# Kernel tuning notes

Hardware: AMD Instinct MI355X
Metric: run time of the kernel (lower is better)

Reference implementation:

```python
import jax, jax.numpy as jnp
import numpy as np

BIT = 64
M_MARGIN = 2.0 * BIT  # m = 2 * bit
ALPHA = 0.1
N_TRAIN = 100000
N_CLASSES = 100
BATCH = 512


def setup_inputs() -> dict:
    key = jax.random.key(0)
    k1, k2, k3, k4 = jax.random.split(key, 4)
    u = jax.random.normal(k1, (BATCH, BIT), dtype=jnp.float32)
    y = jax.random.randint(k2, (BATCH, N_CLASSES), 0, 2).astype(jnp.float32)
    ind = jnp.arange(BATCH, dtype=jnp.int32)
    U = jax.random.normal(k3, (N_TRAIN, BIT), dtype=jnp.float32)
    Y = jax.random.randint(k4, (N_TRAIN, N_CLASSES), 0, 2).astype(jnp.float32)
    return {"u": u, "y": y, "ind": ind, "U": U, "Y": Y}


def reference(u, y, ind, U, Y):
    # Buffer updates (torch uses u.data / y.float(): detached writes)
    U = U.at[ind].set(jax.lax.stop_gradient(u))  # [N, bit]
    Y = Y.at[ind].set(jax.lax.stop_gradient(y))  # [N, C]

    # Pairwise squared L2 distances via the expansion identity (same math as
    # (u[:,None]-U[None]).pow(2).sum(-1) but without the [B,N,bit] intermediate)
    u_sq = jnp.sum(u * u, axis=1, keepdims=True)        # [B, 1]
    U_sq = jnp.sum(U * U, axis=1)[None, :]              # [1, N]
    dist = jnp.maximum(u_sq - 2.0 * (u @ U.T) + U_sq, 0.0)  # [B, N]

    # match mask: 1 where labels share no class (y @ Y.T == 0)
    mismatch = (y @ Y.T == 0).astype(u.dtype)           # [B, N]

    loss = (1.0 - mismatch) * 0.5 * dist + mismatch * 0.5 * jnp.maximum(M_MARGIN - dist, 0.0)
    loss1 = loss.mean()
    loss2 = ALPHA * jnp.abs(1.0 - jnp.sign(u)).mean()
    return loss1 + loss2
```

## Files before the change

### kernel.cpp

```cpp
#include <hip/hip_runtime.h>
#include <stdint.h>

#define NTRAIN 100000
#define BATCH  512
#define BIT    64
#define NCLS   100
#define MARGINF 128.0f

#define CHUNK  256
#define NSCAN  ((NTRAIN + CHUNK - 1) / CHUNK)
#define NCORR  8
#define NGU    2
#define NUS    2
#define LISTCAP 1024

#define YMP_OFF   0
#define YMO_OFF   8192
#define MISS_OFF  16384
#define ACC_OFF   24576
#define CNT_OFF   25600
#define LIST_OFF  25664

typedef unsigned long long u64;

__device__ __forceinline__ uint4 row_mask(const float* __restrict__ row) {
  const float4* r4 = (const float4*)row;
  unsigned w0 = 0, w1 = 0, w2 = 0, w3 = 0;
#pragma unroll
  for (int j = 0; j < NCLS / 4; ++j) {
    float4 v = r4[j];
    int bp = (4 * j) & 31;
    unsigned m = ((v.x != 0.f) ? 1u : 0u) << bp
               | ((v.y != 0.f) ? 2u : 0u) << bp
               | ((v.z != 0.f) ? 4u : 0u) << bp
               | ((v.w != 0.f) ? 8u : 0u) << bp;
    int word = (4 * j) >> 5;
    if (word == 0) w0 |= m; else if (word == 1) w1 |= m;
    else if (word == 2) w2 |= m; else w3 |= m;
  }
  return make_uint4(w0, w1, w2, w3);
}

__device__ __forceinline__ float pair_term(const float* __restrict__ a,
                                           const float* __restrict__ c) {
  const float4* a4 = (const float4*)a;
  const float4* c4 = (const float4*)c;
  float usq = 0.f, Usq = 0.f, uv = 0.f;
#pragma unroll
  for (int k = 0; k < BIT / 4; ++k) {
    float4 x = a4[k], z = c4[k];
    usq = fmaf(x.x, x.x, fmaf(x.y, x.y, fmaf(x.z, x.z, fmaf(x.w, x.w, usq))));
    Usq = fmaf(z.x, z.x, fmaf(z.y, z.y, fmaf(z.z, z.z, fmaf(z.w, z.w, Usq))));
    uv  = fmaf(x.x, z.x, fmaf(x.y, z.y, fmaf(x.z, z.z, fmaf(x.w, z.w, uv))));
  }
  float d = usq + Usq - 2.f * uv;
  float dc = fmaxf(d, 0.f);
  return 0.5f * fmaxf(MARGINF - dc, 0.f) - 0.5f * d;
}

__global__ void __launch_bounds__(64) k_prep(const float* __restrict__ y,
                                             const float* __restrict__ Y,
                                             const int* __restrict__ ind,
                                             uint4* __restrict__ ymaskp,
                                             uint4* __restrict__ ymold,
                                             u64* __restrict__ missg,
                                             float* __restrict__ accf,
                                             int* __restrict__ listcnt) {
  int bid = blockIdx.x, t = threadIdx.x;
  if (bid < 8) {
    int b = bid * 64 + t;
    uint4 ym = row_mask(y + (size_t)b * NCLS);
    ymaskp[b] = ym;
    ymold[b]  = row_mask(Y + (size_t)ind[b] * NCLS);
#pragma unroll
    for (int c = 0; c < NCLS; ++c) {
      unsigned word = (c < 32) ? ym.x : (c < 64) ? ym.y : (c < 96) ? ym.z : ym.w;
      unsigned bit = (word >> (c & 31)) & 1u;
      u64 bal = __ballot(bit == 0u);
      if (t == 0) missg[c * 8 + bid] = bal;
    }
  } else {
    for (int i = t; i < 144; i += 64) accf[i] = 0.0f;
    if (t == 0) *listcnt = 0;
  }
}

__global__ void __launch_bounds__(512) k_main(
    const float4* __restrict__ U4, const float* __restrict__ Uf,
    const float* __restrict__ Y,
    const float4* __restrict__ u4, const float* __restrict__ u,
    const int* __restrict__ ind,
    const uint4* __restrict__ ymaskp, const uint4* __restrict__ ymold,
    const u64* __restrict__ missg,
    float* __restrict__ accf, int* __restrict__ listcnt, int* __restrict__ list) {
  __shared__ uint4 masks[CHUNK];
  __shared__ u64 mlds[NCLS * 9];
  __shared__ float colred[4][64];
  __shared__ float sqred[4];
  int bid = blockIdx.x, t = threadIdx.x;
  int w = t >> 6, l = t & 63;

  if (bid < NSCAN) {
    int n0 = bid * CHUNK;
    int nvalid = min(CHUNK, NTRAIN - n0);
    if (w < 4) {
      masks[t] = (t < nvalid) ? row_mask(Y + (size_t)(n0 + t) * NCLS)
                              : make_uint4(0u, 0u, 0u, 0u);
    } else {
      for (int i = t - 256; i < NCLS * 8; i += 256)
        mlds[(i >> 3) * 9 + (i & 7)] = missg[i];
      float s0 = 0, s1 = 0, s2 = 0, s3 = 0, sq = 0;
      for (int f = t - 256; f < nvalid * (BIT / 4); f += 256) {
        float4 v = U4[(size_t)n0 * (BIT / 4) + f];
        s0 += v.x; s1 += v.y; s2 += v.z; s3 += v.w;
        sq = fmaf(v.x, v.x, fmaf(v.y, v.y, fmaf(v.z, v.z, fmaf(v.w, v.w, sq))));
      }
      s0 += __shfl_xor(s0, 16); s0 += __shfl_xor(s0, 32);
      s1 += __shfl_xor(s1, 16); s1 += __shfl_xor(s1, 32);
      s2 += __shfl_xor(s2, 16); s2 += __shfl_xor(s2, 32);
      s3 += __shfl_xor(s3, 16); s3 += __shfl_xor(s3, 32);
      for (int off = 32; off; off >>= 1) sq += __shfl_xor(sq, off);
      int ww = w - 4;
      if (l < 16) { colred[ww][l * 4 + 0] = s0; colred[ww][l * 4 + 1] = s1;
                    colred[ww][l * 4 + 2] = s2; colred[ww][l * 4 + 3] = s3; }
      if (l == 0) sqred[ww] = sq;
    }
    __syncthreads();
    if (w == 0) {
      atomicAdd(&accf[l], colred[0][l] + colred[1][l] + colred[2][l] + colred[3][l]);
      if (l == 0) atomicAdd(&accf[128], sqred[0] + sqred[1] + sqred[2] + sqred[3]);
    }
    int grp = t >> 3;
    int g   = t & 7;
#pragma unroll
    for (int k = 0; k < CHUNK / 64; ++k) {
      int n_local = grp + 64 * k;
      bool alive = n_local < nvalid;
      uint4 ym = masks[n_local];
      u64 rem0 = (u64)ym.x | ((u64)ym.y << 32);
      u64 rem1 = (u64)ym.z | ((u64)ym.w << 32);
      u64 acc = alive ? ~0ull : 0ull;
      while (__ballot((acc != 0ull) && ((rem0 | rem1) != 0ull)) != 0ull) {
#pragma unroll
        for (int kk = 0; kk < 4; ++kk) {
          int c = -1;
          if (rem0) { c = __builtin_ctzll(rem0); rem0 &= rem0 - 1ull; }
          else if (rem1) { c = 64 + __builtin_ctzll(rem1); rem1 &= rem1 - 1ull; }
          u64 mm = mlds[(c >= 0 ? c : 0) * 9 + g];
          if (c >= 0) acc &= mm;
        }
      }
      u64 mbal = __ballot(acc != 0ull);
      if (g == 0 && ((mbal >> (8 * (grp & 7))) & 0xffull)) {
        int idx = atomicAdd(listcnt, 1);
        if (idx < LISTCAP) list[idx] = n0 + n_local;
      }
    }
  } else if (bid < NSCAN + NCORR) {
    int cb = bid - NSCAN;
    uint4 ym = ymaskp[t];
    float corr = 0.f;
    for (int j = 0; j < 64; ++j) {
      int bp = cb * 64 + j;
      uint4 mo = ymold[bp];
      uint4 mn = ymaskp[bp];
      unsigned a = (ym.x & mo.x) | (ym.y & mo.y) | (ym.z & mo.z) | (ym.w & mo.w);
      unsigned c = (ym.x & mn.x) | (ym.y & mn.y) | (ym.z & mn.z) | (ym.w & mn.w);
      if (__builtin_expect(__ballot((a == 0u) | (c == 0u)) != 0ull, 0)) {
        const float* ub = u + (size_t)t * BIT;
        if (a == 0u) corr -= pair_term(ub, Uf + (size_t)ind[bp] * BIT);
        if (c == 0u) corr += pair_term(ub, u + (size_t)bp * BIT);
      }
    }
    if (corr != 0.f) atomicAdd(&accf[131], corr);
  } else if (bid < NSCAN + NCORR + NGU) {
    int gb = bid - NSCAN - NCORR;
    float s0 = 0, s1 = 0, s2 = 0, s3 = 0, sq = 0;
    for (int f = t; f < 256 * (BIT / 4); f += 512) {
      int r = gb * 256 + (f >> 4);
      float4 v = U4[(size_t)ind[r] * (BIT / 4) + (f & 15)];
      s0 += v.x; s1 += v.y; s2 += v.z; s3 += v.w;
      sq = fmaf(v.x, v.x, fmaf(v.y, v.y, fmaf(v.z, v.z, fmaf(v.w, v.w, sq))));
    }
    s0 += __shfl_xor(s0, 16); s0 += __shfl_xor(s0, 32);
    s1 += __shfl_xor(s1, 16); s1 += __shfl_xor(s1, 32);
    s2 += __shfl_xor(s2, 16); s2 += __shfl_xor(s2, 32);
    s3 += __shfl_xor(s3, 16); s3 += __shfl_xor(s3, 32);
    for (int off = 32; off; off >>= 1) sq += __shfl_xor(sq, off);
    int c4 = l & 15;
    if (l < 16) {
      atomicAdd(&accf[c4 * 4 + 0], -s0); atomicAdd(&accf[c4 * 4 + 1], -s1);
      atomicAdd(&accf[c4 * 4 + 2], -s2); atomicAdd(&accf[c4 * 4 + 3], -s3);
    }
    if (l == 0) atomicAdd(&accf[128], -sq);
  } else {
    int gb = bid - NSCAN - NCORR - NGU;
    float s0 = 0, s1 = 0, s2 = 0, s3 = 0, sq = 0, sg = 0;
    for (int f = t; f < 256 * (BIT / 4); f += 512) {
      float4 v = u4[(size_t)gb * 256 * (BIT / 4) + f];
      s0 += v.x; s1 += v.y; s2 += v.z; s3 += v.w;
      sq = fmaf(v.x, v.x, fmaf(v.y, v.y, fmaf(v.z, v.z, fmaf(v.w, v.w, sq))));
      sg += ((v.x < 0.f) ? 2.f : (v.x == 0.f) ? 1.f : 0.f)
          + ((v.y < 0.f) ? 2.f : (v.y == 0.f) ? 1.f : 0.f)
          + ((v.z < 0.f) ? 2.f : (v.z == 0.f) ? 1.f : 0.f)
          + ((v.w < 0.f) ? 2.f : (v.w == 0.f) ? 1.f : 0.f);
    }
    s0 += __shfl_xor(s0, 16); s0 += __shfl_xor(s0, 32);
    s1 += __shfl_xor(s1, 16); s1 += __shfl_xor(s1, 32);
    s2 += __shfl_xor(s2, 16); s2 += __shfl_xor(s2, 32);
    s3 += __shfl_xor(s3, 16); s3 += __shfl_xor(s3, 32);
    for (int off = 32; off; off >>= 1) { sq += __shfl_xor(sq, off); sg += __shfl_xor(sg, off); }
    int c4 = l & 15;
    if (l < 16) {
      atomicAdd(&accf[64 + c4 * 4 + 0], s0); atomicAdd(&accf[64 + c4 * 4 + 1], s1);
      atomicAdd(&accf[64 + c4 * 4 + 2], s2); atomicAdd(&accf[64 + c4 * 4 + 3], s3);
    }
    if (l == 0) { atomicAdd(&accf[129], sq); atomicAdd(&accf[130], sg); }
  }
}

__global__ void __launch_bounds__(512) k_finalfix(
    const float* __restrict__ Y, const float* __restrict__ u, const float* __restrict__ Uf,
    const uint4* __restrict__ ymaskp, const int* __restrict__ listcnt,
    const int* __restrict__ list, float* __restrict__ accf, float* __restrict__ out) {
  int t = threadIdx.x;
  int cnt = min(*listcnt, LISTCAP);
  if (__builtin_expect(cnt > 0, 0)) {
    uint4 ymb = ymaskp[t];
    float corr = 0.f;
    for (int i = 0; i < cnt; ++i) {
      int n = list[i];
      uint4 Ym = row_mask(Y + (size_t)n * NCLS);
      unsigned m = (ymb.x & Ym.x) | (ymb.y & Ym.y) | (ymb.z & Ym.z) | (ymb.w & Ym.w);
      if (m == 0u) corr += pair_term(u + (size_t)t * BIT, Uf + (size_t)n * BIT);
    }
    if (corr != 0.f) atomicAdd(&accf[131], corr);
  }
  __syncthreads();
  if (t < 64) {
    double dotp = (double)accf[t] * (double)accf[64 + t];
    for (int off = 32; off; off >>= 1) dotp += __shfl_down(dotp, off);
    if (t == 0) {
      double S_Usq = accf[128];
      double s_usq = accf[129];
      double sg    = accf[130];
      double corr  = accf[131];
      double sum_dist = (double)NTRAIN * s_usq + (double)BATCH * S_Usq - 2.0 * dotp;
      double loss1 = (0.5 * sum_dist + corr) / ((double)BATCH * (double)NTRAIN);
      double loss2 = 0.1 * sg / ((double)BATCH * (double)BIT);
      out[0] = (float)(loss1 + loss2);
    }
  }
}

extern "C" void kernel_launch(void* const* d_in, const int* in_sizes, int n_in,
                              void* d_out, int out_size, void* d_ws, size_t ws_size,
                              hipStream_t stream) {
  const float* u   = (const float*)d_in[0];
  const float* y   = (const float*)d_in[1];
  const int*   ind = (const int*)d_in[2];
  const float* U   = (const float*)d_in[3];
  const float* Y   = (const float*)d_in[4];
  uint4* ymaskp = (uint4*)((char*)d_ws + YMP_OFF);
  uint4* ymold  = (uint4*)((char*)d_ws + YMO_OFF);
  u64*   missg  = (u64*)((char*)d_ws + MISS_OFF);
  float* accf   = (float*)((char*)d_ws + ACC_OFF);
  int*   cnt    = (int*)((char*)d_ws + CNT_OFF);
  int*   list   = (int*)((char*)d_ws + LIST_OFF);
  float* out    = (float*)d_out;

  hipLaunchKernelGGL(k_prep, dim3(9), dim3(64), 0, stream,
                     y, Y, ind, ymaskp, ymold, missg, accf, cnt);
  hipLaunchKernelGGL(k_main, dim3(NSCAN + NCORR + NGU + NUS), dim3(512), 0, stream,
                     (const float4*)U, U, Y, (const float4*)u, u, ind,
                     ymaskp, ymold, missg, accf, cnt, list);
  hipLaunchKernelGGL(k_finalfix, dim3(1), dim3(512), 0, stream,
                     Y, u, U, ymaskp, cnt, list, accf, out);
}
```

Before: 127.9 us.

## Coalesce label-mask building with shared-memory atomicOr across all threads

Label bitmasks are now built cooperatively: each thread reads one contiguous float4 of the label matrix and ORs a nibble into a shared-memory mask word, replacing per-row strided loads done by one thread per row. In the main scan kernel all 8 waves now share both the mask build and the U column-sum work, and the prep kernel becomes 2 blocks of 512 threads. The aim is coalesced global reads of Y and better load balance. The cost is shared-memory atomics and integer divides by 25, and the prep kernel's missg construction becomes a serial 64-iteration loop per entry.

```diff
diff --git a/kernel.cpp b/kernel.cpp
--- a/kernel.cpp
+++ b/kernel.cpp
@@ -23,24 +23,6 @@
 
 typedef unsigned long long u64;
 
-__device__ __forceinline__ uint4 row_mask(const float* __restrict__ row) {
-  const float4* r4 = (const float4*)row;
-  unsigned w0 = 0, w1 = 0, w2 = 0, w3 = 0;
-#pragma unroll
-  for (int j = 0; j < NCLS / 4; ++j) {
-    float4 v = r4[j];
-    int bp = (4 * j) & 31;
-    unsigned m = ((v.x != 0.f) ? 1u : 0u) << bp
-               | ((v.y != 0.f) ? 2u : 0u) << bp
-               | ((v.z != 0.f) ? 4u : 0u) << bp
-               | ((v.w != 0.f) ? 8u : 0u) << bp;
-    int word = (4 * j) >> 5;
-    if (word == 0) w0 |= m; else if (word == 1) w1 |= m;
-    else if (word == 2) w2 |= m; else w3 |= m;
-  }
-  return make_uint4(w0, w1, w2, w3);
-}
-
 __device__ __forceinline__ float pair_term(const float* __restrict__ a,
                                            const float* __restrict__ c) {
   const float4* a4 = (const float4*)a;
@@ -58,77 +40,111 @@
   return 0.5f * fmaxf(MARGINF - dc, 0.f) - 0.5f * d;
 }
 
-__global__ void __launch_bounds__(64) k_prep(const float* __restrict__ y,
-                                             const float* __restrict__ Y,
-                                             const int* __restrict__ ind,
-                                             uint4* __restrict__ ymaskp,
-                                             uint4* __restrict__ ymold,
-                                             u64* __restrict__ missg,
-                                             float* __restrict__ accf,
-                                             int* __restrict__ listcnt) {
+__device__ __forceinline__ unsigned nib4(float4 v) {
+  return ((v.x != 0.f) ? 1u : 0u) | ((v.y != 0.f) ? 2u : 0u)
+       | ((v.z != 0.f) ? 4u : 0u) | ((v.w != 0.f) ? 8u : 0u);
+}
+
+__global__ void __launch_bounds__(512) k_prep(const float4* __restrict__ y4,
+                                              const float4* __restrict__ Y4,
+                                              const int* __restrict__ ind,
+                                              uint4* __restrict__ ymaskp,
+                                              uint4* __restrict__ ymold,
+                                              u64* __restrict__ missg,
+                                              float* __restrict__ accf,
+                                              int* __restrict__ listcnt) {
+  __shared__ __align__(16) unsigned mw[BATCH][4];
+  __shared__ int indl[BATCH];
   int bid = blockIdx.x, t = threadIdx.x;
-  if (bid < 8) {
-    int b = bid * 64 + t;
-    uint4 ym = row_mask(y + (size_t)b * NCLS);
-    ymaskp[b] = ym;
-    ymold[b]  = row_mask(Y + (size_t)ind[b] * NCLS);
-#pragma unroll
-    for (int c = 0; c < NCLS; ++c) {
-      unsigned word = (c < 32) ? ym.x : (c < 64) ? ym.y : (c < 96) ? ym.z : ym.w;
-      unsigned bit = (word >> (c & 31)) & 1u;
-      u64 bal = __ballot(bit == 0u);
-      if (t == 0) missg[c * 8 + bid] = bal;
+  ((uint4*)mw)[t] = make_uint4(0u, 0u, 0u, 0u);
+  if (bid == 1) indl[t] = ind[t];
+  __syncthreads();
+
+  if (bid == 0) {
+    for (int f = t; f < BATCH * 25; f += 512) {
+      float4 v = y4[f];
+      int row = f / 25, q = f - row * 25;
+      unsigned s = 4u * (unsigned)q;
+      atomicOr(&mw[row][s >> 5], nib4(v) << (s & 31u));
+    }
+    __syncthreads();
+    ((uint4*)ymaskp)[t] = ((const uint4*)mw)[t];
+    for (int un = t; un < 8 * NCLS; un += 512) {
+      int g = un / NCLS, c = un - (un / NCLS) * NCLS;
+      u64 m = 0;
+      for (int j = 0; j < 64; ++j) {
+        unsigned wrd = mw[g * 64 + j][c >> 5];
+        if (!((wrd >> (c & 31)) & 1u)) m |= 1ull << j;
+      }
+      missg[(size_t)c * 8 + g] = m;
     }
   } else {
-    for (int i = t; i < 144; i += 64) accf[i] = 0.0f;
-    if (t == 0) *listcnt = 0;
+    for (int f = t; f < BATCH * 25; f += 512) {
+      int row = f / 25, q = f - row * 25;
+      float4 v = Y4[(size_t)indl[row] * 25 + q];
+      unsigned s = 4u * (unsigned)q;
+      atomicOr(&mw[row][s >> 5], nib4(v) << (s & 31u));
+    }
+    __syncthreads();
+    ((uint4*)ymold)[t] = ((const uint4*)mw)[t];
+    if (t < 144) accf[t] = 0.0f;
+    if (t == 200) *listcnt = 0;
   }
 }
 
 __global__ void __launch_bounds__(512) k_main(
     const float4* __restrict__ U4, const float* __restrict__ Uf,
-    const float* __restrict__ Y,
+    const float4* __restrict__ Y4,
     const float4* __restrict__ u4, const float* __restrict__ u,
     const int* __restrict__ ind,
     const uint4* __restrict__ ymaskp, const uint4* __restrict__ ymold,
     const u64* __restrict__ missg,
     float* __restrict__ accf, int* __restrict__ listcnt, int* __restrict__ list) {
-  __shared__ uint4 masks[CHUNK];
+  __shared__ __align__(16) unsigned masksw[CHUNK][4];
   __shared__ u64 mlds[NCLS * 9];
-  __shared__ float colred[4][64];
-  __shared__ float sqred[4];
+  __shared__ float colred[8][64];
+  __shared__ float sqred[8];
   int bid = blockIdx.x, t = threadIdx.x;
   int w = t >> 6, l = t & 63;
 
   if (bid < NSCAN) {
     int n0 = bid * CHUNK;
     int nvalid = min(CHUNK, NTRAIN - n0);
-    if (w < 4) {
-      masks[t] = (t < nvalid) ? row_mask(Y + (size_t)(n0 + t) * NCLS)
-                              : make_uint4(0u, 0u, 0u, 0u);
-    } else {
-      for (int i = t - 256; i < NCLS * 8; i += 256)
-        mlds[(i >> 3) * 9 + (i & 7)] = missg[i];
-      float s0 = 0, s1 = 0, s2 = 0, s3 = 0, sq = 0;
-      for (int f = t - 256; f < nvalid * (BIT / 4); f += 256) {
-        float4 v = U4[(size_t)n0 * (BIT / 4) + f];
-        s0 += v.x; s1 += v.y; s2 += v.z; s3 += v.w;
-        sq = fmaf(v.x, v.x, fmaf(v.y, v.y, fmaf(v.z, v.z, fmaf(v.w, v.w, sq))));
-      }
-      s0 += __shfl_xor(s0, 16); s0 += __shfl_xor(s0, 32);
-      s1 += __shfl_xor(s1, 16); s1 += __shfl_xor(s1, 32);
-      s2 += __shfl_xor(s2, 16); s2 += __shfl_xor(s2, 32);
-      s3 += __shfl_xor(s3, 16); s3 += __shfl_xor(s3, 32);
-      for (int off = 32; off; off >>= 1) sq += __shfl_xor(sq, off);
-      int ww = w - 4;
-      if (l < 16) { colred[ww][l * 4 + 0] = s0; colred[ww][l * 4 + 1] = s1;
-                    colred[ww][l * 4 + 2] = s2; colred[ww][l * 4 + 3] = s3; }
-      if (l == 0) sqred[ww] = sq;
-    }
+    if (t < CHUNK) ((uint4*)masksw)[t] = make_uint4(0u, 0u, 0u, 0u);
+    for (int i = t; i < NCLS * 8; i += 512)
+      mlds[(i >> 3) * 9 + (i & 7)] = missg[i];
+    __syncthreads();
+    for (int f = t; f < nvalid * 25; f += 512) {
+      float4 v = Y4[(size_t)n0 * 25 + f];
+      int row = f / 25, q = f - row * 25;
+      unsigned s = 4u * (unsigned)q;
+      atomicOr(&masksw[row][s >> 5], nib4(v) << (s & 31u));
+    }
+    float s0 = 0, s1 = 0, s2 = 0, s3 = 0, sq = 0;
+    for (int f = t; f < nvalid * (BIT / 4); f += 512) {
+      float4 v = U4[(size_t)n0 * (BIT / 4) + f];
+      s0 += v.x; s1 += v.y; s2 += v.z; s3 += v.w;
+      sq = fmaf(v.x, v.x, fmaf(v.y, v.y, fmaf(v.z, v.z, fmaf(v.w, v.w, sq))));
+    }
+    s0 += __shfl_xor(s0, 16); s0 += __shfl_xor(s0, 32);
+    s1 += __shfl_xor(s1, 16); s1 += __shfl_xor(s1, 32);
+    s2 += __shfl_xor(s2, 16); s2 += __shfl_xor(s2, 32);
+    s3 += __shfl_xor(s3, 16); s3 += __shfl_xor(s3, 32);
+    for (int off = 32; off; off >>= 1) sq += __shfl_xor(sq, off);
+    if (l < 16) { colred[w][l * 4 + 0] = s0; colred[w][l * 4 + 1] = s1;
+                  colred[w][l * 4 + 2] = s2; colred[w][l * 4 + 3] = s3; }
+    if (l == 0) sqred[w] = sq;
     __syncthreads();
     if (w == 0) {
-      atomicAdd(&accf[l], colred[0][l] + colred[1][l] + colred[2][l] + colred[3][l]);
-      if (l == 0) atomicAdd(&accf[128], sqred[0] + sqred[1] + sqred[2] + sqred[3]);
+      float cs = 0, qs = 0;
+#pragma unroll
+      for (int ww = 0; ww < 8; ++ww) cs += colred[ww][l];
+      atomicAdd(&accf[l], cs);
+      if (l == 0) {
+#pragma unroll
+        for (int ww = 0; ww < 8; ++ww) qs += sqred[ww];
+        atomicAdd(&accf[128], qs);
+      }
     }
     int grp = t >> 3;
     int g   = t & 7;
@@ -136,7 +152,7 @@
     for (int k = 0; k < CHUNK / 64; ++k) {
       int n_local = grp + 64 * k;
       bool alive = n_local < nvalid;
-      uint4 ym = masks[n_local];
+      uint4 ym = ((const uint4*)masksw)[n_local];
       u64 rem0 = (u64)ym.x | ((u64)ym.y << 32);
       u64 rem1 = (u64)ym.z | ((u64)ym.w << 32);
       u64 acc = alive ? ~0ull : 0ull;
@@ -230,8 +246,15 @@
     float corr = 0.f;
     for (int i = 0; i < cnt; ++i) {
       int n = list[i];
-      uint4 Ym = row_mask(Y + (size_t)n * NCLS);
-      unsigned m = (ymb.x & Ym.x) | (ymb.y & Ym.y) | (ymb.z & Ym.z) | (ymb.w & Ym.w);
+      const float* row = Y + (size_t)n * NCLS;
+      unsigned w0 = 0, w1 = 0, w2 = 0, w3 = 0;
+      for (int c = 0; c < NCLS; ++c) {
+        if (row[c] != 0.f) {
+          if (c < 32) w0 |= 1u << c; else if (c < 64) w1 |= 1u << (c - 32);
+          else if (c < 96) w2 |= 1u << (c - 64); else w3 |= 1u << (c - 96);
+        }
+      }
+      unsigned m = (ymb.x & w0) | (ymb.y & w1) | (ymb.z & w2) | (ymb.w & w3);
       if (m == 0u) corr += pair_term(u + (size_t)t * BIT, Uf + (size_t)n * BIT);
     }
     if (corr != 0.f) atomicAdd(&accf[131], corr);
@@ -269,10 +292,10 @@
   int*   list   = (int*)((char*)d_ws + LIST_OFF);
   float* out    = (float*)d_out;
 
-  hipLaunchKernelGGL(k_prep, dim3(9), dim3(64), 0, stream,
-                     y, Y, ind, ymaskp, ymold, missg, accf, cnt);
+  hipLaunchKernelGGL(k_prep, dim3(2), dim3(512), 0, stream,
+                     (const float4*)y, (const float4*)Y, ind, ymaskp, ymold, missg, accf, cnt);
   hipLaunchKernelGGL(k_main, dim3(NSCAN + NCORR + NGU + NUS), dim3(512), 0, stream,
-                     (const float4*)U, U, Y, (const float4*)u, u, ind,
+                     (const float4*)U, U, (const float4*)Y, (const float4*)u, u, ind,
                      ymaskp, ymold, missg, accf, cnt, list);
   hipLaunchKernelGGL(k_finalfix, dim3(1), dim3(512), 0, stream,
                      Y, u, U, ymaskp, cnt, list, accf, out);
```

Result: slower. 131.7 us (median of 2 runs) (+2.9%).

## Split fused scan into streaming mask/sum kernel and separate brute-force screening kernel

Applied to the files above, without the earlier changes.

The single fused main kernel is split in two. A new streaming kernel converts Y rows to bitmasks (32 lanes per row, combined with shuffle-OR) and writes them to a workspace array, while other blocks compute the column sums of U with a grid-stride loop. A second kernel then screens each 128-row chunk by brute force: every batch row is ANDed against every chunk mask, which replaces the per-class ballot intersection loop and the missg table. This adds a kernel launch and a global round-trip of the 100k×16-byte mask array, in exchange for fully coalesced streaming and simpler screening.

```diff
diff --git a/kernel.cpp b/kernel.cpp
--- a/kernel.cpp
+++ b/kernel.cpp
@@ -7,33 +7,37 @@
 #define NCLS   100
 #define MARGINF 128.0f
 
-#define CHUNK  256
-#define NSCAN  ((NTRAIN + CHUNK - 1) / CHUNK)
-#define NCORR  8
-#define NGU    2
-#define NUS    2
+typedef unsigned long long u64;
+
+#define YB   608
+#define UB   384
+#define USB  2
+#define GSB  2
+#define KA_BLOCKS (YB + UB + USB + GSB)
+
+#define CHUNKB  128
+#define NSCANB  ((NTRAIN + CHUNKB - 1) / CHUNKB)
+#define NCORR   8
 #define LISTCAP 1024
 
 #define YMP_OFF   0
 #define YMO_OFF   8192
-#define MISS_OFF  16384
-#define ACC_OFF   24576
-#define CNT_OFF   25600
-#define LIST_OFF  25664
-
-typedef unsigned long long u64;
+#define ACC_OFF   16384
+#define CNT_OFF   17408
+#define LIST_OFF  17472
+#define YMASK_OFF 32768
+
+__device__ __forceinline__ unsigned nib4(float4 v) {
+  return ((v.x != 0.f) ? 1u : 0u) | ((v.y != 0.f) ? 2u : 0u)
+       | ((v.z != 0.f) ? 4u : 0u) | ((v.w != 0.f) ? 8u : 0u);
+}
 
 __device__ __forceinline__ uint4 row_mask(const float* __restrict__ row) {
   const float4* r4 = (const float4*)row;
   unsigned w0 = 0, w1 = 0, w2 = 0, w3 = 0;
 #pragma unroll
   for (int j = 0; j < NCLS / 4; ++j) {
-    float4 v = r4[j];
-    int bp = (4 * j) & 31;
-    unsigned m = ((v.x != 0.f) ? 1u : 0u) << bp
-               | ((v.y != 0.f) ? 2u : 0u) << bp
-               | ((v.z != 0.f) ? 4u : 0u) << bp
-               | ((v.w != 0.f) ? 8u : 0u) << bp;
+    unsigned m = nib4(r4[j]) << ((4 * j) & 31);
     int word = (4 * j) >> 5;
     if (word == 0) w0 |= m; else if (word == 1) w1 |= m;
     else if (word == 2) w2 |= m; else w3 |= m;
@@ -58,106 +62,158 @@
   return 0.5f * fmaxf(MARGINF - dc, 0.f) - 0.5f * d;
 }
 
-__global__ void __launch_bounds__(64) k_prep(const float* __restrict__ y,
-                                             const float* __restrict__ Y,
-                                             const int* __restrict__ ind,
-                                             uint4* __restrict__ ymaskp,
-                                             uint4* __restrict__ ymold,
-                                             u64* __restrict__ missg,
-                                             float* __restrict__ accf,
-                                             int* __restrict__ listcnt) {
-  int bid = blockIdx.x, t = threadIdx.x;
-  if (bid < 8) {
-    int b = bid * 64 + t;
-    uint4 ym = row_mask(y + (size_t)b * NCLS);
-    ymaskp[b] = ym;
-    ymold[b]  = row_mask(Y + (size_t)ind[b] * NCLS);
-#pragma unroll
-    for (int c = 0; c < NCLS; ++c) {
-      unsigned word = (c < 32) ? ym.x : (c < 64) ? ym.y : (c < 96) ? ym.z : ym.w;
-      unsigned bit = (word >> (c & 31)) & 1u;
-      u64 bal = __ballot(bit == 0u);
-      if (t == 0) missg[c * 8 + bid] = bal;
-    }
-  } else {
-    for (int i = t; i < 144; i += 64) accf[i] = 0.0f;
-    if (t == 0) *listcnt = 0;
-  }
-}
-
-__global__ void __launch_bounds__(512) k_main(
-    const float4* __restrict__ U4, const float* __restrict__ Uf,
-    const float* __restrict__ Y,
-    const float4* __restrict__ u4, const float* __restrict__ u,
-    const int* __restrict__ ind,
-    const uint4* __restrict__ ymaskp, const uint4* __restrict__ ymold,
-    const u64* __restrict__ missg,
-    float* __restrict__ accf, int* __restrict__ listcnt, int* __restrict__ list) {
-  __shared__ uint4 masks[CHUNK];
-  __shared__ u64 mlds[NCLS * 9];
-  __shared__ float colred[4][64];
-  __shared__ float sqred[4];
+__global__ void __launch_bounds__(512) k_prep(const float* __restrict__ y,
+                                              const float* __restrict__ Y,
+                                              const int* __restrict__ ind,
+                                              uint4* __restrict__ ymaskp,
+                                              uint4* __restrict__ ymold,
+                                              float* __restrict__ accf,
+                                              int* __restrict__ listcnt) {
+  int t = threadIdx.x;
+  ymaskp[t] = row_mask(y + (size_t)t * NCLS);
+  ymold[t]  = row_mask(Y + (size_t)ind[t] * NCLS);
+  if (t < 144) accf[t] = 0.0f;
+  if (t == 200) *listcnt = 0;
+}
+
+__global__ void __launch_bounds__(256) k_stream(const float4* __restrict__ Y4,
+                                                const float4* __restrict__ U4,
+                                                const float4* __restrict__ u4,
+                                                const int* __restrict__ ind,
+                                                uint4* __restrict__ Ymask,
+                                                float* __restrict__ accf) {
   int bid = blockIdx.x, t = threadIdx.x;
   int w = t >> 6, l = t & 63;
 
-  if (bid < NSCAN) {
-    int n0 = bid * CHUNK;
-    int nvalid = min(CHUNK, NTRAIN - n0);
-    if (w < 4) {
-      masks[t] = (t < nvalid) ? row_mask(Y + (size_t)(n0 + t) * NCLS)
-                              : make_uint4(0u, 0u, 0u, 0u);
-    } else {
-      for (int i = t - 256; i < NCLS * 8; i += 256)
-        mlds[(i >> 3) * 9 + (i & 7)] = missg[i];
-      float s0 = 0, s1 = 0, s2 = 0, s3 = 0, sq = 0;
-      for (int f = t - 256; f < nvalid * (BIT / 4); f += 256) {
-        float4 v = U4[(size_t)n0 * (BIT / 4) + f];
-        s0 += v.x; s1 += v.y; s2 += v.z; s3 += v.w;
-        sq = fmaf(v.x, v.x, fmaf(v.y, v.y, fmaf(v.z, v.z, fmaf(v.w, v.w, sq))));
+  if (bid < YB) {
+    int grp = (bid << 3) | (t >> 5);
+    int q = t & 31;
+    int wi = q >> 3;
+    for (int r = grp; r < NTRAIN; r += YB * 8) {
+      unsigned nib = 0;
+      if (q < 25) nib = nib4(Y4[(size_t)r * 25 + q]) << ((4 * q) & 31);
+      unsigned w0 = (q < 25 && wi == 0) ? nib : 0u;
+      unsigned w1 = (q < 25 && wi == 1) ? nib : 0u;
+      unsigned w2 = (q < 25 && wi == 2) ? nib : 0u;
+      unsigned w3 = (q < 25 && wi == 3) ? nib : 0u;
+#pragma unroll
+      for (int d = 1; d < 32; d <<= 1) {
+        w0 |= __shfl_xor(w0, d); w1 |= __shfl_xor(w1, d);
+        w2 |= __shfl_xor(w2, d); w3 |= __shfl_xor(w3, d);
       }
-      s0 += __shfl_xor(s0, 16); s0 += __shfl_xor(s0, 32);
-      s1 += __shfl_xor(s1, 16); s1 += __shfl_xor(s1, 32);
-      s2 += __shfl_xor(s2, 16); s2 += __shfl_xor(s2, 32);
-      s3 += __shfl_xor(s3, 16); s3 += __shfl_xor(s3, 32);
-      for (int off = 32; off; off >>= 1) sq += __shfl_xor(sq, off);
-      int ww = w - 4;
-      if (l < 16) { colred[ww][l * 4 + 0] = s0; colred[ww][l * 4 + 1] = s1;
-                    colred[ww][l * 4 + 2] = s2; colred[ww][l * 4 + 3] = s3; }
-      if (l == 0) sqred[ww] = sq;
-    }
+      if (q == 0) Ymask[r] = make_uint4(w0, w1, w2, w3);
+    }
+  } else if (bid < YB + UB) {
+    const int TOT = UB * 256;
+    int tid = (bid - YB) * 256 + t;
+    float s0 = 0, s1 = 0, s2 = 0, s3 = 0, sq = 0;
+    for (int f = tid; f < NTRAIN * (BIT / 4); f += TOT) {
+      float4 v = U4[f];
+      s0 += v.x; s1 += v.y; s2 += v.z; s3 += v.w;
+      sq = fmaf(v.x, v.x, fmaf(v.y, v.y, fmaf(v.z, v.z, fmaf(v.w, v.w, sq))));
+    }
+    s0 += __shfl_xor(s0, 16); s0 += __shfl_xor(s0, 32);
+    s1 += __shfl_xor(s1, 16); s1 += __shfl_xor(s1, 32);
+    s2 += __shfl_xor(s2, 16); s2 += __shfl_xor(s2, 32);
+    s3 += __shfl_xor(s3, 16); s3 += __shfl_xor(s3, 32);
+    for (int off = 32; off; off >>= 1) sq += __shfl_xor(sq, off);
+    __shared__ float colred[4][64];
+    __shared__ float sqred[4];
+    if (l < 16) { colred[w][l * 4 + 0] = s0; colred[w][l * 4 + 1] = s1;
+                  colred[w][l * 4 + 2] = s2; colred[w][l * 4 + 3] = s3; }
+    if (l == 0) sqred[w] = sq;
     __syncthreads();
     if (w == 0) {
       atomicAdd(&accf[l], colred[0][l] + colred[1][l] + colred[2][l] + colred[3][l]);
       if (l == 0) atomicAdd(&accf[128], sqred[0] + sqred[1] + sqred[2] + sqred[3]);
     }
-    int grp = t >> 3;
-    int g   = t & 7;
-#pragma unroll
-    for (int k = 0; k < CHUNK / 64; ++k) {
-      int n_local = grp + 64 * k;
-      bool alive = n_local < nvalid;
-      uint4 ym = masks[n_local];
-      u64 rem0 = (u64)ym.x | ((u64)ym.y << 32);
-      u64 rem1 = (u64)ym.z | ((u64)ym.w << 32);
-      u64 acc = alive ? ~0ull : 0ull;
-      while (__ballot((acc != 0ull) && ((rem0 | rem1) != 0ull)) != 0ull) {
-#pragma unroll
-        for (int kk = 0; kk < 4; ++kk) {
-          int c = -1;
-          if (rem0) { c = __builtin_ctzll(rem0); rem0 &= rem0 - 1ull; }
-          else if (rem1) { c = 64 + __builtin_ctzll(rem1); rem1 &= rem1 - 1ull; }
-          u64 mm = mlds[(c >= 0 ? c : 0) * 9 + g];
-          if (c >= 0) acc &= mm;
-        }
+  } else if (bid < YB + UB + USB) {
+    int tid = (bid - YB - UB) * 256 + t;
+    float s0 = 0, s1 = 0, s2 = 0, s3 = 0, sq = 0, sg = 0;
+    for (int f = tid; f < BATCH * (BIT / 4); f += USB * 256) {
+      float4 v = u4[f];
+      s0 += v.x; s1 += v.y; s2 += v.z; s3 += v.w;
+      sq = fmaf(v.x, v.x, fmaf(v.y, v.y, fmaf(v.z, v.z, fmaf(v.w, v.w, sq))));
+      sg += ((v.x < 0.f) ? 2.f : (v.x == 0.f) ? 1.f : 0.f)
+          + ((v.y < 0.f) ? 2.f : (v.y == 0.f) ? 1.f : 0.f)
+          + ((v.z < 0.f) ? 2.f : (v.z == 0.f) ? 1.f : 0.f)
+          + ((v.w < 0.f) ? 2.f : (v.w == 0.f) ? 1.f : 0.f);
+    }
+    s0 += __shfl_xor(s0, 16); s0 += __shfl_xor(s0, 32);
+    s1 += __shfl_xor(s1, 16); s1 += __shfl_xor(s1, 32);
+    s2 += __shfl_xor(s2, 16); s2 += __shfl_xor(s2, 32);
+    s3 += __shfl_xor(s3, 16); s3 += __shfl_xor(s3, 32);
+    for (int off = 32; off; off >>= 1) { sq += __shfl_xor(sq, off); sg += __shfl_xor(sg, off); }
+    int c4 = l & 15;
+    if (l < 16) {
+      atomicAdd(&accf[64 + c4 * 4 + 0], s0); atomicAdd(&accf[64 + c4 * 4 + 1], s1);
+      atomicAdd(&accf[64 + c4 * 4 + 2], s2); atomicAdd(&accf[64 + c4 * 4 + 3], s3);
+    }
+    if (l == 0) { atomicAdd(&accf[129], sq); atomicAdd(&accf[130], sg); }
+  } else {
+    int tid = (bid - YB - UB - USB) * 256 + t;
+    float s0 = 0, s1 = 0, s2 = 0, s3 = 0, sq = 0;
+    for (int f = tid; f < BATCH * (BIT / 4); f += GSB * 256) {
+      float4 v = U4[(size_t)ind[f >> 4] * (BIT / 4) + (f & 15)];
+      s0 += v.x; s1 += v.y; s2 += v.z; s3 += v.w;
+      sq = fmaf(v.x, v.x, fmaf(v.y, v.y, fmaf(v.z, v.z, fmaf(v.w, v.w, sq))));
+    }
+    s0 += __shfl_xor(s0, 16); s0 += __shfl_xor(s0, 32);
+    s1 += __shfl_xor(s1, 16); s1 += __shfl_xor(s1, 32);
+    s2 += __shfl_xor(s2, 16); s2 += __shfl_xor(s2, 32);
+    s3 += __shfl_xor(s3, 16); s3 += __shfl_xor(s3, 32);
+    for (int off = 32; off; off >>= 1) sq += __shfl_xor(sq, off);
+    int c4 = l & 15;
+    if (l < 16) {
+      atomicAdd(&accf[c4 * 4 + 0], -s0); atomicAdd(&accf[c4 * 4 + 1], -s1);
+      atomicAdd(&accf[c4 * 4 + 2], -s2); atomicAdd(&accf[c4 * 4 + 3], -s3);
+    }
+    if (l == 0) atomicAdd(&accf[128], -sq);
+  }
+}
+
+__global__ void __launch_bounds__(512) k_screen(const uint4* __restrict__ Ymask,
+                                                const uint4* __restrict__ ymaskp,
+                                                const uint4* __restrict__ ymold,
+                                                const float* __restrict__ u,
+                                                const float* __restrict__ Uf,
+                                                const int* __restrict__ ind,
+                                                float* __restrict__ accf,
+                                                int* __restrict__ listcnt,
+                                                int* __restrict__ list) {
+  int bid = blockIdx.x, t = threadIdx.x;
+  if (bid < NSCANB) {
+    __shared__ uint4 masks[CHUNKB];
+    __shared__ unsigned char hits[CHUNKB];
+    int n0 = bid * CHUNKB;
+    int nvalid = min(CHUNKB, NTRAIN - n0);
+    if (t < CHUNKB) {
+      masks[t] = (t < nvalid) ? Ymask[n0 + t] : make_uint4(~0u, ~0u, ~0u, ~0u);
+      hits[t] = 0;
+    }
+    __syncthreads();
+    uint4 ym = ymaskp[t];
+    unsigned anyhit = 0u;
+#pragma unroll 2
+    for (int j = 0; j < CHUNKB; ++j) {
+      uint4 Ym = masks[j];
+      unsigned m = (ym.x & Ym.x) | (ym.y & Ym.y) | (ym.z & Ym.z) | (ym.w & Ym.w);
+      anyhit |= (m == 0u) ? 1u : 0u;
+    }
+    if (__builtin_expect(__ballot(anyhit != 0u) != 0ull, 0)) {
+      for (int j = 0; j < CHUNKB; ++j) {
+        uint4 Ym = masks[j];
+        unsigned m = (ym.x & Ym.x) | (ym.y & Ym.y) | (ym.z & Ym.z) | (ym.w & Ym.w);
+        if (m == 0u) hits[j] = 1;
       }
-      u64 mbal = __ballot(acc != 0ull);
-      if (g == 0 && ((mbal >> (8 * (grp & 7))) & 0xffull)) {
-        int idx = atomicAdd(listcnt, 1);
-        if (idx < LISTCAP) list[idx] = n0 + n_local;
-      }
-    }
-  } else if (bid < NSCAN + NCORR) {
-    int cb = bid - NSCAN;
+    }
+    __syncthreads();
+    if (t < nvalid && hits[t]) {
+      int idx = atomicAdd(listcnt, 1);
+      if (idx < LISTCAP) list[idx] = n0 + t;
+    }
+  } else {
+    int cb = bid - NSCANB;
     uint4 ym = ymaskp[t];
     float corr = 0.f;
     for (int j = 0; j < 64; ++j) {
@@ -173,49 +229,6 @@
       }
     }
     if (corr != 0.f) atomicAdd(&accf[131], corr);
-  } else if (bid < NSCAN + NCORR + NGU) {
-    int gb = bid - NSCAN - NCORR;
-    float s0 = 0, s1 = 0, s2 = 0, s3 = 0, sq = 0;
-    for (int f = t; f < 256 * (BIT / 4); f += 512) {
-      int r = gb * 256 + (f >> 4);
-      float4 v = U4[(size_t)ind[r] * (BIT / 4) + (f & 15)];
-      s0 += v.x; s1 += v.y; s2 += v.z; s3 += v.w;
-      sq = fmaf(v.x, v.x, fmaf(v.y, v.y, fmaf(v.z, v.z, fmaf(v.w, v.w, sq))));
-    }
-    s0 += __shfl_xor(s0, 16); s0 += __shfl_xor(s0, 32);
-    s1 += __shfl_xor(s1, 16); s1 += __shfl_xor(s1, 32);
-    s2 += __shfl_xor(s2, 16); s2 += __shfl_xor(s2, 32);
-    s3 += __shfl_xor(s3, 16); s3 += __shfl_xor(s3, 32);
-    for (int off = 32; off; off >>= 1) sq += __shfl_xor(sq, off);
-    int c4 = l & 15;
-    if (l < 16) {
-      atomicAdd(&accf[c4 * 4 + 0], -s0); atomicAdd(&accf[c4 * 4 + 1], -s1);
-      atomicAdd(&accf[c4 * 4 + 2], -s2); atomicAdd(&accf[c4 * 4 + 3], -s3);
-    }
-    if (l == 0) atomicAdd(&accf[128], -sq);
-  } else {
-    int gb = bid - NSCAN - NCORR - NGU;
-    float s0 = 0, s1 = 0, s2 = 0, s3 = 0, sq = 0, sg = 0;
-    for (int f = t; f < 256 * (BIT / 4); f += 512) {
-      float4 v = u4[(size_t)gb * 256 * (BIT / 4) + f];
-      s0 += v.x; s1 += v.y; s2 += v.z; s3 += v.w;
-      sq = fmaf(v.x, v.x, fmaf(v.y, v.y, fmaf(v.z, v.z, fmaf(v.w, v.w, sq))));
-      sg += ((v.x < 0.f) ? 2.f : (v.x == 0.f) ? 1.f : 0.f)
-          + ((v.y < 0.f) ? 2.f : (v.y == 0.f) ? 1.f : 0.f)
-          + ((v.z < 0.f) ? 2.f : (v.z == 0.f) ? 1.f : 0.f)
-          + ((v.w < 0.f) ? 2.f : (v.w == 0.f) ? 1.f : 0.f);
-    }
-    s0 += __shfl_xor(s0, 16); s0 += __shfl_xor(s0, 32);
-    s1 += __shfl_xor(s1, 16); s1 += __shfl_xor(s1, 32);
-    s2 += __shfl_xor(s2, 16); s2 += __shfl_xor(s2, 32);
-    s3 += __shfl_xor(s3, 16); s3 += __shfl_xor(s3, 32);
-    for (int off = 32; off; off >>= 1) { sq += __shfl_xor(sq, off); sg += __shfl_xor(sg, off); }
-    int c4 = l & 15;
-    if (l < 16) {
-      atomicAdd(&accf[64 + c4 * 4 + 0], s0); atomicAdd(&accf[64 + c4 * 4 + 1], s1);
-      atomicAdd(&accf[64 + c4 * 4 + 2], s2); atomicAdd(&accf[64 + c4 * 4 + 3], s3);
-    }
-    if (l == 0) { atomicAdd(&accf[129], sq); atomicAdd(&accf[130], sg); }
   }
 }
 
@@ -263,17 +276,18 @@
   const float* Y   = (const float*)d_in[4];
   uint4* ymaskp = (uint4*)((char*)d_ws + YMP_OFF);
   uint4* ymold  = (uint4*)((char*)d_ws + YMO_OFF);
-  u64*   missg  = (u64*)((char*)d_ws + MISS_OFF);
   float* accf   = (float*)((char*)d_ws + ACC_OFF);
   int*   cnt    = (int*)((char*)d_ws + CNT_OFF);
   int*   list   = (int*)((char*)d_ws + LIST_OFF);
+  uint4* Ymask  = (uint4*)((char*)d_ws + YMASK_OFF);
   float* out    = (float*)d_out;
 
-  hipLaunchKernelGGL(k_prep, dim3(9), dim3(64), 0, stream,
-                     y, Y, ind, ymaskp, ymold, missg, accf, cnt);
-  hipLaunchKernelGGL(k_main, dim3(NSCAN + NCORR + NGU + NUS), dim3(512), 0, stream,
-                     (const float4*)U, U, Y, (const float4*)u, u, ind,
-                     ymaskp, ymold, missg, accf, cnt, list);
+  hipLaunchKernelGGL(k_prep, dim3(1), dim3(512), 0, stream,
+                     y, Y, ind, ymaskp, ymold, accf, cnt);
+  hipLaunchKernelGGL(k_stream, dim3(KA_BLOCKS), dim3(256), 0, stream,
+                     (const float4*)Y, (const float4*)U, (const float4*)u, ind, Ymask, accf);
+  hipLaunchKernelGGL(k_screen, dim3(NSCANB + NCORR), dim3(512), 0, stream,
+                     Ymask, ymaskp, ymold, u, U, ind, accf, cnt, list);
   hipLaunchKernelGGL(k_finalfix, dim3(1), dim3(512), 0, stream,
                      Y, u, U, ymaskp, cnt, list, accf, out);
 }
```

Result: slower. 155.0 us (+21.2%).
